# Performance work log

Hardware: AMD Instinct MI355X
Metric: run time of the kernel (lower is better)

The kernel has to match this reference:

```python
import jax, jax.numpy as jnp
import numpy as np

N, E = 16384, 262144
IN, H, OUT = 128, 256, 256
L, HEADS = 4, 8
OC = H // HEADS  # 32, also MHA head_dim
B, NB = 64, 256  # graphs, nodes per graph (N = B*NB, equal-size graphs)


def _ln(x, g, b, eps=1e-5):
    m = x.mean(-1, keepdims=True)
    v = ((x - m) ** 2).mean(-1, keepdims=True)
    return (x - m) / jnp.sqrt(v + eps) * g + b


def setup_inputs() -> dict:
    key = jax.random.key(0)
    ks = iter(jax.random.split(key, 40))
    r = lambda *s: jax.random.normal(next(ks), s, jnp.float32) * 0.05
    return dict(
        x=jax.random.normal(next(ks), (N, IN), jnp.float32),
        edge_index=jax.random.randint(next(ks), (2, E), 0, N),
        wi=r(IN, H), bi=r(H),
        wg=r(L, H, H), asrc=r(L, HEADS, OC), adst=r(L, HEADS, OC), bg=r(L, H),
        g1=jnp.ones((L, H)), b1=jnp.zeros((L, H)),
        inw=r(L, 3 * H, H), inb=r(L, 3 * H), ow=r(L, H, H), ob=r(L, H),
        g2=jnp.ones((L, H)), b2=jnp.zeros((L, H)),
        mw1=r(L, H, 2 * H), mb1=r(L, 2 * H), mw2=r(L, 2 * H, H), mb2=r(L, H),
        g3=jnp.ones((L, H)), b3=jnp.zeros((L, H)),
        gf=jnp.ones(H), bf=jnp.zeros(H),
        wo=r(H, OUT), bo=r(OUT),
    )


def reference(x, edge_index, wi, bi, wg, asrc, adst, bg, g1, b1, inw, inb,
              ow, ob, g2, b2, mw1, mb1, mw2, mb2, g3, b3, gf, bf, wo, bo):
    src, dst = edge_index[0], edge_index[1]
    x = jax.nn.relu(x @ wi + bi)  # [N, H]
    for i in range(L):
        # ---- GATConv (local MPNN), eval mode (no dropout) ----
        xw = (x @ wg[i]).reshape(N, HEADS, OC)
        a = (xw * asrc[i]).sum(-1)[src] + (xw * adst[i]).sum(-1)[dst]  # [E, HEADS]
        a = jax.nn.leaky_relu(a, 0.2)
        amax = jax.ops.segment_max(a, dst, num_segments=N)
        ae = jnp.exp(a - amax[dst])
        asum = jax.ops.segment_sum(ae, dst, num_segments=N)
        attn = ae / asum[dst]  # edge softmax per destination node
        h = jax.ops.segment_sum(attn[:, :, None] * xw[src], dst, num_segments=N)
        h = h.reshape(N, H) + bg[i]
        h = _ln(h + x, g1[i], b1[i])  # GPSConv local branch + residual + norm1
        # ---- global MultiheadAttention over dense batch (equal-size graphs) ----
        xd = x.reshape(B, NB, H)
        qkv = xd @ inw[i].T + inb[i]
        q, k, v = jnp.split(qkv, 3, axis=-1)
        q = q.reshape(B, NB, HEADS, OC).transpose(0, 2, 1, 3)
        k = k.reshape(B, NB, HEADS, OC).transpose(0, 2, 1, 3)
        v = v.reshape(B, NB, HEADS, OC).transpose(0, 2, 1, 3)
        p = jax.nn.softmax(jnp.einsum('bhqd,bhkd->bhqk', q, k) / jnp.sqrt(jnp.float32(OC)), axis=-1)
        o = jnp.einsum('bhqk,bhkd->bhqd', p, v).transpose(0, 2, 1, 3).reshape(B, NB, H)
        o = (o @ ow[i].T + ob[i]).reshape(N, H)
        h2 = _ln(o + x, g2[i], b2[i])  # global branch + residual + norm2
        out = h + h2
        out = out + (jax.nn.relu(out @ mw1[i] + mb1[i]) @ mw2[i] + mb2[i])  # MLP residual
        x = _ln(out, g3[i], b3[i])  # norm3
    x = _ln(x, gf, bf)
    return x @ wo + bo
```

## Files before the change

### kernel.cpp

```cpp
#include <hip/hip_runtime.h>
#include <hip/hip_bf16.h>

#define NNODES 16384
#define NEDGES 262144
#define IND    128
#define HD     256
#define OUTDIM 256
#define LAYERS 4
#define NHEADS 8
#define OCD    32
#define NGRAPH 64
#define NBATCH 256
#define XQSTR  1024

typedef __hip_bfloat16 bf16;
typedef __attribute__((ext_vector_type(8))) short bf16x8;
typedef __attribute__((ext_vector_type(4))) short s16x4;
typedef __attribute__((ext_vector_type(4))) float f32x4;

__device__ __forceinline__ short bfbits(float v) {
    bf16 h = __float2bfloat16(v);
    return *(short*)&h;
}
__device__ __forceinline__ float b2f(short s) {
    return __uint_as_float(((unsigned)(unsigned short)s) << 16);
}

__device__ __forceinline__ void gload_lds16(const short* g, short* l) {
    __builtin_amdgcn_global_load_lds(
        (const __attribute__((address_space(1))) void*)g,
        (__attribute__((address_space(3))) void*)l, 16, 0, 0);
}

__global__ void cvt_kernel(const float* __restrict__ in, short* __restrict__ out, int n)
{
    int i = blockIdx.x * blockDim.x + threadIdx.x;
    if (i < n) out[i] = bfbits(in[i]);
}

__global__ void transpose_cvt_kernel(const float* __restrict__ in, short* __restrict__ out,
                                     int K, int N)
{
    int i = blockIdx.x * blockDim.x + threadIdx.x;
    if (i >= K * N) return;
    const float* ip = in + (size_t)blockIdx.y * K * N;
    short* op = out + (size_t)blockIdx.y * K * N;
    int k = i / N, n = i % N;
    op[(size_t)n * K + k] = bfbits(ip[i]);
}

__global__ void build_wcomb_kernel(const float* __restrict__ inw, const float* __restrict__ wg,
                                   short* __restrict__ wcomb)
{
    int i = blockIdx.x * blockDim.x + threadIdx.x;
    int l = i >> 18, r = (i >> 8) & 1023, k = i & 255;
    float v;
    if (r < 768) v = inw[(size_t)l * 768 * 256 + r * 256 + k];
    else         v = wg[(size_t)l * 256 * 256 + k * 256 + (r - 768)];
    wcomb[i] = bfbits(v);
}

__global__ void build_cbias_kernel(const float* __restrict__ inb, float* __restrict__ cbias)
{
    int i = blockIdx.x * blockDim.x + threadIdx.x;
    int l = i >> 10, c = i & 1023;
    cbias[i] = (c < 768) ? inb[l * 768 + c] : 0.f;
}

__global__ void hist_kernel(const int* __restrict__ dst, int* __restrict__ cnt)
{
    int e = blockIdx.x * blockDim.x + threadIdx.x;
    if (e < NEDGES) atomicAdd(&cnt[dst[e]], 1);
}

__global__ void scan_kernel(const int* __restrict__ cnt, int* __restrict__ row_ptr)
{
    __shared__ int part[256];
    int t = threadIdx.x;
    const int PER = NNODES / 256;
    int base = t * PER;
    int s = 0;
    for (int i = 0; i < PER; i++) s += cnt[base + i];
    part[t] = s;
    __syncthreads();
    for (int off = 1; off < 256; off <<= 1) {
        int v = (t >= off) ? part[t - off] : 0;
        __syncthreads();
        part[t] += v;
        __syncthreads();
    }
    int run = (t == 0) ? 0 : part[t - 1];
    for (int i = 0; i < PER; i++) { row_ptr[base + i] = run; run += cnt[base + i]; }
    if (t == 255) row_ptr[NNODES] = run;
}

__global__ void scatter_kernel(const int* __restrict__ src, const int* __restrict__ dst,
                               const int* __restrict__ row_ptr, int* __restrict__ fill,
                               int* __restrict__ srcs)
{
    int e = blockIdx.x * blockDim.x + threadIdx.x;
    if (e >= NEDGES) return;
    int d = dst[e];
    int pos = row_ptr[d] + atomicAdd(&fill[d], 1);
    srcs[pos] = src[e];
}

__global__ void gat_scores_kernel(const short* __restrict__ xw16,
                                  const float* __restrict__ asrc, const float* __restrict__ adst,
                                  float* __restrict__ ssrc, float* __restrict__ sdst)
{
    int i = blockIdx.x * blockDim.x + threadIdx.x;
    if (i >= NNODES * NHEADS) return;
    int n = i >> 3, h = i & 7;
    const bf16x8* xr = (const bf16x8*)(xw16 + (size_t)n * XQSTR + h * OCD);
    float s1 = 0.f, s2 = 0.f;
#pragma unroll
    for (int g = 0; g < 4; g++) {
        bf16x8 v8 = xr[g];
#pragma unroll
        for (int j = 0; j < 8; j++) {
            float v = b2f(v8[j]);
            int d = g * 8 + j;
            s1 += v * asrc[h * OCD + d];
            s2 += v * adst[h * OCD + d];
        }
    }
    ssrc[i] = s1;
    sdst[i] = s2;
}

__global__ __launch_bounds__(256)
void gat_agg_ln_kernel(const int* __restrict__ row_ptr, const int* __restrict__ srcs,
                       const float* __restrict__ ssrc, const float* __restrict__ sdst,
                       const short* __restrict__ xw16, const float* __restrict__ xcur,
                       const float* __restrict__ colbias, const float* __restrict__ gamma,
                       const float* __restrict__ beta, float* __restrict__ out)
{
    int wave = threadIdx.x >> 6, lane = threadIdx.x & 63;
    int n = blockIdx.x * 4 + wave;
    int c0 = lane << 2;
    int h = c0 >> 5;
    int start = row_ptr[n];
    int deg = row_ptr[n + 1] - start;
    float sd = sdst[n * NHEADS + h];

    float ax = 0.f, ay = 0.f, az = 0.f, aw = 0.f, l = 0.f;
    int j = 0;
    for (; j + 4 <= deg; j += 4) {
        int e0 = srcs[start + j + 0], e1 = srcs[start + j + 1];
        int e2 = srcs[start + j + 2], e3 = srcs[start + j + 3];
        s16x4 r0 = *(const s16x4*)&xw16[(size_t)e0 * XQSTR + c0];
        s16x4 r1 = *(const s16x4*)&xw16[(size_t)e1 * XQSTR + c0];
        s16x4 r2 = *(const s16x4*)&xw16[(size_t)e2 * XQSTR + c0];
        s16x4 r3 = *(const s16x4*)&xw16[(size_t)e3 * XQSTR + c0];
        float a0 = ssrc[e0 * NHEADS + h] + sd; a0 = a0 > 0.f ? a0 : 0.2f * a0;
        float a1 = ssrc[e1 * NHEADS + h] + sd; a1 = a1 > 0.f ? a1 : 0.2f * a1;
        float a2 = ssrc[e2 * NHEADS + h] + sd; a2 = a2 > 0.f ? a2 : 0.2f * a2;
        float a3 = ssrc[e3 * NHEADS + h] + sd; a3 = a3 > 0.f ? a3 : 0.2f * a3;
        float p0 = __expf(a0), p1 = __expf(a1), p2 = __expf(a2), p3 = __expf(a3);
        l += (p0 + p1) + (p2 + p3);
        ax += p0 * b2f(r0[0]) + p1 * b2f(r1[0]) + p2 * b2f(r2[0]) + p3 * b2f(r3[0]);
        ay += p0 * b2f(r0[1]) + p1 * b2f(r1[1]) + p2 * b2f(r2[1]) + p3 * b2f(r3[1]);
        az += p0 * b2f(r0[2]) + p1 * b2f(r1[2]) + p2 * b2f(r2[2]) + p3 * b2f(r3[2]);
        aw += p0 * b2f(r0[3]) + p1 * b2f(r1[3]) + p2 * b2f(r2[3]) + p3 * b2f(r3[3]);
    }
    for (; j < deg; j++) {
        int e0 = srcs[start + j];
        s16x4 r0 = *(const s16x4*)&xw16[(size_t)e0 * XQSTR + c0];
        float a0 = ssrc[e0 * NHEADS + h] + sd; a0 = a0 > 0.f ? a0 : 0.2f * a0;
        float p0 = __expf(a0);
        l += p0;
        ax += p0 * b2f(r0[0]); ay += p0 * b2f(r0[1]);
        az += p0 * b2f(r0[2]); aw += p0 * b2f(r0[3]);
    }
    float invl = deg ? 1.f / l : 0.f;
    size_t base = (size_t)n * HD + c0;
    float4 x4 = *(const float4*)&xcur[base];
    float4 cb = *(const float4*)&colbias[c0];
    float4 v;
    v.x = ax * invl + x4.x + cb.x;
    v.y = ay * invl + x4.y + cb.y;
    v.z = az * invl + x4.z + cb.z;
    v.w = aw * invl + x4.w + cb.w;
    float s = v.x + v.y + v.z + v.w;
    float q = v.x * v.x + v.y * v.y + v.z * v.z + v.w * v.w;
#pragma unroll
    for (int off = 1; off < 64; off <<= 1) {
        s += __shfl_xor(s, off);
        q += __shfl_xor(q, off);
    }
    float mean = s * (1.f / HD);
    float var  = fmaxf(q * (1.f / HD) - mean * mean, 0.f);
    float inv  = rsqrtf(var + 1e-5f);
    float4 g  = *(const float4*)&gamma[c0];
    float4 bt = *(const float4*)&beta[c0];
    float4 y;
    y.x = (v.x - mean) * inv * g.x + bt.x;
    y.y = (v.y - mean) * inv * g.y + bt.y;
    y.z = (v.z - mean) * inv * g.z + bt.z;
    y.w = (v.w - mean) * inv * g.w + bt.w;
    *(float4*)&out[base] = y;
}

#define GBM 128
#define GBK 32

template<int TN>
__global__ __launch_bounds__(256)
void gemm_mfma_kernel(const short* __restrict__ A16, const short* __restrict__ B16,
                      const float* __restrict__ bias, const float* __restrict__ resid,
                      float* __restrict__ Cf, short* __restrict__ C16,
                      int M, int Nc, int K, int relu)
{
    constexpr int NTF = TN / 32;
    __shared__ short As[GBM * GBK];
    __shared__ short Bs[TN * GBK];
    int tid = threadIdx.x;
    int wid = tid >> 6, lane = tid & 63;
    int quad = lane >> 4, l16 = lane & 15;
    int wm = wid >> 1, wn = wid & 1;
    int rowBase = blockIdx.y * GBM;
    int colBase = blockIdx.x * TN;

    f32x4 acc[4][NTF];
#pragma unroll
    for (int mt = 0; mt < 4; mt++)
#pragma unroll
        for (int nt = 0; nt < NTF; nt++) acc[mt][nt] = (f32x4)(0.f);

    int ar  = tid >> 2;
    int akq = (tid & 3) * 8;

    const short* Ag0 = &A16[(size_t)(rowBase + ar) * K + akq];
    const short* Ag1 = &A16[(size_t)(rowBase + ar + 64) * K + akq];
    const short* Bg0 = &B16[(size_t)(colBase + ar) * K + akq];
    const short* Bg1 = (TN == 128) ? &B16[(size_t)(colBase + ar + 64) * K + akq] : nullptr;
    short* AsW0 = As + wid * 512;
    short* AsW1 = As + 64 * GBK + wid * 512;
    short* BsW0 = Bs + wid * 512;
    short* BsW1 = Bs + 64 * GBK + wid * 512;

    for (int k0 = 0; k0 < K; k0 += GBK) {
        gload_lds16(Ag0 + k0, AsW0);
        gload_lds16(Ag1 + k0, AsW1);
        gload_lds16(Bg0 + k0, BsW0);
        if (TN == 128) gload_lds16(Bg1 + k0, BsW1);
        __syncthreads();
        bf16x8 aF[4], bF[NTF];
#pragma unroll
        for (int mt = 0; mt < 4; mt++)
            aF[mt] = *(bf16x8*)&As[(wm * 64 + mt * 16 + l16) * GBK + quad * 8];
#pragma unroll
        for (int nt = 0; nt < NTF; nt++)
            bF[nt] = *(bf16x8*)&Bs[(wn * (TN / 2) + nt * 16 + l16) * GBK + quad * 8];
#pragma unroll
        for (int mt = 0; mt < 4; mt++)
#pragma unroll
            for (int nt = 0; nt < NTF; nt++)
                acc[mt][nt] = __builtin_amdgcn_mfma_f32_16x16x32_bf16(
                    aF[mt], bF[nt], acc[mt][nt], 0, 0, 0);
        __syncthreads();
    }

#pragma unroll
    for (int mt = 0; mt < 4; mt++) {
#pragma unroll
        for (int nt = 0; nt < NTF; nt++) {
            int col = colBase + wn * (TN / 2) + nt * 16 + l16;
            float bv = bias ? bias[col] : 0.f;
#pragma unroll
            for (int r = 0; r < 4; r++) {
                int row = rowBase + wm * 64 + mt * 16 + quad * 4 + r;
                float v = acc[mt][nt][r] + bv;
                if (resid) v += resid[(size_t)row * Nc + col];
                if (relu)  v = fmaxf(v, 0.f);
                if (Cf)  Cf[(size_t)row * Nc + col] = v;
                if (C16) C16[(size_t)row * Nc + col] = bfbits(v);
            }
        }
    }
}

__global__ __launch_bounds__(256)
void ln4_kernel(const float* __restrict__ in, const float* __restrict__ res,
                const float* __restrict__ gamma, const float* __restrict__ beta,
                const float* __restrict__ postadd,
                float* __restrict__ outf, short* __restrict__ out16)
{
    int wave = threadIdx.x >> 6, lane = threadIdx.x & 63;
    int row = blockIdx.x * 4 + wave;
    size_t base = (size_t)row * HD + lane * 4;
    float4 v = *(const float4*)&in[base];
    if (res) {
        float4 r = *(const float4*)&res[base];
        v.x += r.x; v.y += r.y; v.z += r.z; v.w += r.w;
    }
    float s = v.x + v.y + v.z + v.w;
    float q = v.x * v.x + v.y * v.y + v.z * v.z + v.w * v.w;
#pragma unroll
    for (int off = 1; off < 64; off <<= 1) {
        s += __shfl_xor(s, off);
        q += __shfl_xor(q, off);
    }
    float mean = s * (1.f / HD);
    float var  = fmaxf(q * (1.f / HD) - mean * mean, 0.f);
    float inv  = rsqrtf(var + 1e-5f);
    float4 g  = *(const float4*)&gamma[lane * 4];
    float4 bt = *(const float4*)&beta[lane * 4];
    float4 y;
    y.x = (v.x - mean) * inv * g.x + bt.x;
    y.y = (v.y - mean) * inv * g.y + bt.y;
    y.z = (v.z - mean) * inv * g.z + bt.z;
    y.w = (v.w - mean) * inv * g.w + bt.w;
    if (postadd) {
        float4 p = *(const float4*)&postadd[base];
        y.x += p.x; y.y += p.y; y.z += p.z; y.w += p.w;
    }
    if (outf) *(float4*)&outf[base] = y;
    if (out16) {
        s16x4 o;
        o[0] = bfbits(y.x); o[1] = bfbits(y.y); o[2] = bfbits(y.z); o[3] = bfbits(y.w);
        *(s16x4*)&out16[base] = o;
    }
}

#define PSTR 72
__global__ __launch_bounds__(256)
void mha_mfma_kernel(const short* __restrict__ qkv16, short* __restrict__ o16)
{
    __shared__ short smem[4 * 64 * PSTR + 32 * PSTR];
    short* VT = smem + 4 * 64 * PSTR;

    int b = blockIdx.x, h = blockIdx.y;
    int tid = threadIdx.x;
    int wid = tid >> 6, lane = tid & 63;
    int quad = lane >> 4, l16 = lane & 15;
    int base = b * NBATCH;
    int qrow0 = wid * 64;
    short* Pme = smem + wid * 64 * PSTR;

    const float scale2 = 0.17677669529663687f * 1.4426950408889634f;

    bf16x8 qA[4];
#pragma unroll
    for (int mt = 0; mt < 4; mt++)
        qA[mt] = *(const bf16x8*)&qkv16[(size_t)(base + qrow0 + mt * 16 + l16) * XQSTR + h * 32 + quad * 8];

    f32x4 accO[4][2];
#pragma unroll
    for (int mt = 0; mt < 4; mt++)
#pragma unroll
        for (int dt = 0; dt < 2; dt++) accO[mt][dt] = (f32x4)(0.f);
    float lsum[4][4];
#pragma unroll
    for (int mt = 0; mt < 4; mt++)
#pragma unroll
        for (int r = 0; r < 4; r++) lsum[mt][r] = 0.f;

    for (int c = 0; c < 4; c++) {
        __syncthreads();
        {
            int key = tid >> 2, dq = (tid & 3) * 8;
            bf16x8 v = *(const bf16x8*)&qkv16[(size_t)(base + c * 64 + key) * XQSTR + 512 + h * 32 + dq];
#pragma unroll
            for (int j = 0; j < 8; j++) VT[(dq + j) * PSTR + key] = v[j];
        }
        __syncthreads();
        bf16x8 kB[4];
#pragma unroll
        for (int kt = 0; kt < 4; kt++)
            kB[kt] = *(const bf16x8*)&qkv16[(size_t)(base + c * 64 + kt * 16 + l16) * XQSTR + 256 + h * 32 + quad * 8];
#pragma unroll
        for (int mt = 0; mt < 4; mt++) {
#pragma unroll
            for (int kt = 0; kt < 4; kt++) {
                f32x4 s = __builtin_amdgcn_mfma_f32_16x16x32_bf16(qA[mt], kB[kt], (f32x4)(0.f), 0, 0, 0);
#pragma unroll
                for (int r = 0; r < 4; r++) {
                    float p = exp2f(s[r] * scale2);
                    lsum[mt][r] += p;
                    Pme[(mt * 16 + quad * 4 + r) * PSTR + kt * 16 + l16] = bfbits(p);
                }
            }
        }
        __syncthreads();
#pragma unroll
        for (int mt = 0; mt < 4; mt++) {
#pragma unroll
            for (int ks = 0; ks < 2; ks++) {
                bf16x8 pA = *(bf16x8*)&Pme[(mt * 16 + l16) * PSTR + ks * 32 + quad * 8];
#pragma unroll
                for (int dt = 0; dt < 2; dt++) {
                    bf16x8 vB = *(bf16x8*)&VT[(dt * 16 + l16) * PSTR + ks * 32 + quad * 8];
                    accO[mt][dt] = __builtin_amdgcn_mfma_f32_16x16x32_bf16(pA, vB, accO[mt][dt], 0, 0, 0);
                }
            }
        }
    }
#pragma unroll
    for (int mt = 0; mt < 4; mt++)
#pragma unroll
        for (int r = 0; r < 4; r++) {
            float v = lsum[mt][r];
            v += __shfl_xor(v, 1);
            v += __shfl_xor(v, 2);
            v += __shfl_xor(v, 4);
            v += __shfl_xor(v, 8);
            lsum[mt][r] = v;
        }
#pragma unroll
    for (int mt = 0; mt < 4; mt++)
#pragma unroll
        for (int dt = 0; dt < 2; dt++)
#pragma unroll
            for (int r = 0; r < 4; r++) {
                int row = base + qrow0 + mt * 16 + quad * 4 + r;
                int col = h * 32 + dt * 16 + l16;
                o16[(size_t)row * HD + col] = bfbits(accO[mt][dt][r] / lsum[mt][r]);
            }
}

extern "C" void kernel_launch(void* const* d_in, const int* in_sizes, int n_in,
                              void* d_out, int out_size, void* d_ws, size_t ws_size,
                              hipStream_t stream)
{
    const float* x0   = (const float*)d_in[0];
    const int*   ei   = (const int*)d_in[1];
    const float* wi   = (const float*)d_in[2];
    const float* bi   = (const float*)d_in[3];
    const float* wg   = (const float*)d_in[4];
    const float* asrc = (const float*)d_in[5];
    const float* adst = (const float*)d_in[6];
    const float* bg   = (const float*)d_in[7];
    const float* g1   = (const float*)d_in[8];
    const float* b1   = (const float*)d_in[9];
    const float* inw  = (const float*)d_in[10];
    const float* inb  = (const float*)d_in[11];
    const float* ow   = (const float*)d_in[12];
    const float* ob   = (const float*)d_in[13];
    const float* g2   = (const float*)d_in[14];
    const float* b2   = (const float*)d_in[15];
    const float* mw1  = (const float*)d_in[16];
    const float* mb1  = (const float*)d_in[17];
    const float* mw2  = (const float*)d_in[18];
    const float* mb2  = (const float*)d_in[19];
    const float* g3   = (const float*)d_in[20];
    const float* b3   = (const float*)d_in[21];
    const float* gf   = (const float*)d_in[22];
    const float* bf_  = (const float*)d_in[23];
    const float* wo   = (const float*)d_in[24];
    const float* bo   = (const float*)d_in[25];

    const int* srcI = ei;
    const int* dstI = ei + NEDGES;

    const size_t NH = (size_t)NNODES * HD;
    float* ws   = (float*)d_ws;
    float* xcur = ws;
    float* xw   = xcur + NH;
    float* hbuf = xw + NH;
    float* obuf = hbuf + NH;
    float* qkvb = obuf + NH;
    int*   srcs    = (int*)(qkvb + 3 * NH);
    int*   row_ptr = srcs + NEDGES;
    int*   cnt     = row_ptr + NNODES + 1;
    int*   fill    = cnt + NNODES;
    float* ssrc    = (float*)(fill + NNODES);
    float* sdst    = ssrc + (size_t)NNODES * NHEADS;
    short* xq16   = (short*)qkvb;
    short* x016   = (short*)(sdst + (size_t)NNODES * NHEADS);
    short* xcur16 = x016 + (size_t)NNODES * IND;
    short* b16a   = xcur16 + NH;
    short* hid16  = b16a + NH;
    short* wi_t  = hid16 + 2 * NH;
    short* wcomb = wi_t + (size_t)HD * IND;
    short* ow_c  = wcomb + (size_t)LAYERS * 1024 * HD;
    short* mw1_t = ow_c + (size_t)LAYERS * HD * HD;
    short* mw2_t = mw1_t + (size_t)LAYERS * HD * 2 * HD;
    short* wo_t  = mw2_t + (size_t)LAYERS * 2 * HD * HD;
    float* cbias = (float*)(wo_t + (size_t)HD * OUTDIM);

    const int T = 256;
    const int nNH = NNODES * NHEADS;

    cvt_kernel<<<(NNODES * IND + T - 1) / T, T, 0, stream>>>(x0, x016, NNODES * IND);
    transpose_cvt_kernel<<<dim3((IND * HD + T - 1) / T, 1), T, 0, stream>>>(wi, wi_t, IND, HD);
    build_wcomb_kernel<<<(LAYERS * 1024 * HD) / T, T, 0, stream>>>(inw, wg, wcomb);
    build_cbias_kernel<<<(LAYERS * 1024) / T, T, 0, stream>>>(inb, cbias);
    cvt_kernel<<<(LAYERS * HD * HD + T - 1) / T, T, 0, stream>>>(ow, ow_c, LAYERS * HD * HD);
    transpose_cvt_kernel<<<dim3((HD * 2 * HD + T - 1) / T, LAYERS), T, 0, stream>>>(mw1, mw1_t, HD, 2 * HD);
    transpose_cvt_kernel<<<dim3((2 * HD * HD + T - 1) / T, LAYERS), T, 0, stream>>>(mw2, mw2_t, 2 * HD, HD);
    transpose_cvt_kernel<<<dim3((HD * OUTDIM + T - 1) / T, 1), T, 0, stream>>>(wo, wo_t, HD, OUTDIM);

    hipMemsetAsync(cnt, 0, NNODES * sizeof(int), stream);
    hipMemsetAsync(fill, 0, NNODES * sizeof(int), stream);
    hist_kernel<<<(NEDGES + T - 1) / T, T, 0, stream>>>(dstI, cnt);
    scan_kernel<<<1, 256, 0, stream>>>(cnt, row_ptr);
    scatter_kernel<<<(NEDGES + T - 1) / T, T, 0, stream>>>(srcI, dstI, row_ptr, fill, srcs);

    gemm_mfma_kernel<64><<<dim3(HD / 64, NNODES / GBM), 256, 0, stream>>>(
        x016, wi_t, bi, nullptr, xcur, xcur16, NNODES, HD, IND, 1);

    for (int i = 0; i < LAYERS; i++) {
        const float* asrc_i = asrc + (size_t)i * NHEADS * OCD;
        const float* adst_i = adst + (size_t)i * NHEADS * OCD;
        const float* bg_i   = bg + (size_t)i * HD;
        const float* g1_i   = g1 + (size_t)i * HD;
        const float* b1_i   = b1 + (size_t)i * HD;
        const float* ob_i   = ob + (size_t)i * HD;
        const float* g2_i   = g2 + (size_t)i * HD;
        const float* b2_i   = b2 + (size_t)i * HD;
        const float* mb1_i  = mb1 + (size_t)i * 2 * HD;
        const float* mb2_i  = mb2 + (size_t)i * HD;
        const float* g3_i   = g3 + (size_t)i * HD;
        const float* b3_i   = b3 + (size_t)i * HD;
        const short* wcomb_i = wcomb + (size_t)i * 1024 * HD;
        const float* cbias_i = cbias + (size_t)i * 1024;
        const short* ow_ci  = ow_c + (size_t)i * HD * HD;
        const short* mw1_ti = mw1_t + (size_t)i * HD * 2 * HD;
        const short* mw2_ti = mw2_t + (size_t)i * 2 * HD * HD;

        gemm_mfma_kernel<128><<<dim3(1024 / 128, NNODES / GBM), 256, 0, stream>>>(
            xcur16, wcomb_i, cbias_i, nullptr, nullptr, xq16, NNODES, 1024, HD, 0);

        gat_scores_kernel<<<(nNH + T - 1) / T, T, 0, stream>>>(xq16 + 768, asrc_i, adst_i, ssrc, sdst);
        gat_agg_ln_kernel<<<NNODES / 4, 256, 0, stream>>>(
            row_ptr, srcs, ssrc, sdst, xq16 + 768, xcur, bg_i, g1_i, b1_i, hbuf);

        mha_mfma_kernel<<<dim3(NGRAPH, NHEADS), 256, 0, stream>>>(xq16, b16a);
        gemm_mfma_kernel<64><<<dim3(HD / 64, NNODES / GBM), 256, 0, stream>>>(
            b16a, ow_ci, ob_i, nullptr, xw, nullptr, NNODES, HD, HD, 0);
        ln4_kernel<<<NNODES / 4, 256, 0, stream>>>(xw, xcur, g2_i, b2_i, hbuf, obuf, b16a);

        gemm_mfma_kernel<128><<<dim3(2 * HD / 128, NNODES / GBM), 256, 0, stream>>>(
            b16a, mw1_ti, mb1_i, nullptr, nullptr, hid16, NNODES, 2 * HD, HD, 1);
        gemm_mfma_kernel<64><<<dim3(HD / 64, NNODES / GBM), 256, 0, stream>>>(
            hid16, mw2_ti, mb2_i, obuf, xw, nullptr, NNODES, HD, 2 * HD, 0);
        ln4_kernel<<<NNODES / 4, 256, 0, stream>>>(xw, nullptr, g3_i, b3_i, nullptr, xcur, xcur16);
    }

    ln4_kernel<<<NNODES / 4, 256, 0, stream>>>(xcur, nullptr, gf, bf_, nullptr, nullptr, b16a);
    gemm_mfma_kernel<64><<<dim3(OUTDIM / 64, NNODES / GBM), 256, 0, stream>>>(
        b16a, wo_t, bo, nullptr, (float*)d_out, nullptr, NNODES, OUTDIM, HD, 0);
}
```

Measured before the change: 879.3 us.

## Fuse output-projection and MLP-down GEMMs with LayerNorm epilogue, vectorize GEMM stores

```diff
diff --git a/kernel.cpp b/kernel.cpp
--- a/kernel.cpp
+++ b/kernel.cpp
@@ -258,25 +258,158 @@
 #pragma unroll
             for (int nt = 0; nt < NTF; nt++)
                 acc[mt][nt] = __builtin_amdgcn_mfma_f32_16x16x32_bf16(
-                    aF[mt], bF[nt], acc[mt][nt], 0, 0, 0);
+                    bF[nt], aF[mt], acc[mt][nt], 0, 0, 0);
         __syncthreads();
     }
 
 #pragma unroll
     for (int mt = 0; mt < 4; mt++) {
+        int row = rowBase + wm * 64 + mt * 16 + l16;
 #pragma unroll
         for (int nt = 0; nt < NTF; nt++) {
-            int col = colBase + wn * (TN / 2) + nt * 16 + l16;
-            float bv = bias ? bias[col] : 0.f;
-#pragma unroll
-            for (int r = 0; r < 4; r++) {
-                int row = rowBase + wm * 64 + mt * 16 + quad * 4 + r;
-                float v = acc[mt][nt][r] + bv;
-                if (resid) v += resid[(size_t)row * Nc + col];
-                if (relu)  v = fmaxf(v, 0.f);
-                if (Cf)  Cf[(size_t)row * Nc + col] = v;
-                if (C16) C16[(size_t)row * Nc + col] = bfbits(v);
-            }
+            int col0 = colBase + wn * (TN / 2) + nt * 16 + quad * 4;
+            f32x4 v = acc[mt][nt];
+            if (bias) {
+                float4 b4 = *(const float4*)&bias[col0];
+                v[0] += b4.x; v[1] += b4.y; v[2] += b4.z; v[3] += b4.w;
+            }
+            if (resid) {
+                float4 r4 = *(const float4*)&resid[(size_t)row * Nc + col0];
+                v[0] += r4.x; v[1] += r4.y; v[2] += r4.z; v[3] += r4.w;
+            }
+            if (relu) {
+                v[0] = fmaxf(v[0], 0.f); v[1] = fmaxf(v[1], 0.f);
+                v[2] = fmaxf(v[2], 0.f); v[3] = fmaxf(v[3], 0.f);
+            }
+            if (Cf) {
+                float4 o; o.x = v[0]; o.y = v[1]; o.z = v[2]; o.w = v[3];
+                *(float4*)&Cf[(size_t)row * Nc + col0] = o;
+            }
+            if (C16) {
+                s16x4 o;
+                o[0] = bfbits(v[0]); o[1] = bfbits(v[1]);
+                o[2] = bfbits(v[2]); o[3] = bfbits(v[3]);
+                *(s16x4*)&C16[(size_t)row * Nc + col0] = o;
+            }
+        }
+    }
+}
+
+__global__ __launch_bounds__(256)
+void gemm_ln_kernel(const short* __restrict__ A16, const short* __restrict__ B16,
+                    const float* __restrict__ bias, const float* __restrict__ resid,
+                    const float* __restrict__ gamma, const float* __restrict__ beta,
+                    const float* __restrict__ postadd,
+                    float* __restrict__ outf, short* __restrict__ out16, int K)
+{
+    __shared__ short As[GBM * GBK];
+    __shared__ short Bs[256 * GBK];
+    __shared__ float sred_s[2][GBM];
+    __shared__ float sred_q[2][GBM];
+    int tid = threadIdx.x;
+    int wid = tid >> 6, lane = tid & 63;
+    int quad = lane >> 4, l16 = lane & 15;
+    int wm = wid >> 1, wn = wid & 1;
+    int rowBase = blockIdx.y * GBM;
+
+    f32x4 acc[4][8];
+#pragma unroll
+    for (int mt = 0; mt < 4; mt++)
+#pragma unroll
+        for (int nt = 0; nt < 8; nt++) acc[mt][nt] = (f32x4)(0.f);
+
+    int ar  = tid >> 2;
+    int akq = (tid & 3) * 8;
+
+    const short* Ag0 = &A16[(size_t)(rowBase + ar) * K + akq];
+    const short* Ag1 = &A16[(size_t)(rowBase + ar + 64) * K + akq];
+    const short* Bg0 = &B16[(size_t)(ar) * K + akq];
+    const short* Bg1 = &B16[(size_t)(ar + 64) * K + akq];
+    const short* Bg2 = &B16[(size_t)(ar + 128) * K + akq];
+    const short* Bg3 = &B16[(size_t)(ar + 192) * K + akq];
+    short* AsW0 = As + wid * 512;
+    short* AsW1 = As + 64 * GBK + wid * 512;
+    short* BsW0 = Bs + wid * 512;
+    short* BsW1 = Bs + 64 * GBK + wid * 512;
+    short* BsW2 = Bs + 128 * GBK + wid * 512;
+    short* BsW3 = Bs + 192 * GBK + wid * 512;
+
+    for (int k0 = 0; k0 < K; k0 += GBK) {
+        gload_lds16(Ag0 + k0, AsW0);
+        gload_lds16(Ag1 + k0, AsW1);
+        gload_lds16(Bg0 + k0, BsW0);
+        gload_lds16(Bg1 + k0, BsW1);
+        gload_lds16(Bg2 + k0, BsW2);
+        gload_lds16(Bg3 + k0, BsW3);
+        __syncthreads();
+        bf16x8 aF[4], bF[8];
+#pragma unroll
+        for (int mt = 0; mt < 4; mt++)
+            aF[mt] = *(bf16x8*)&As[(wm * 64 + mt * 16 + l16) * GBK + quad * 8];
+#pragma unroll
+        for (int nt = 0; nt < 8; nt++)
+            bF[nt] = *(bf16x8*)&Bs[(wn * 128 + nt * 16 + l16) * GBK + quad * 8];
+#pragma unroll
+        for (int mt = 0; mt < 4; mt++)
+#pragma unroll
+            for (int nt = 0; nt < 8; nt++)
+                acc[mt][nt] = __builtin_amdgcn_mfma_f32_16x16x32_bf16(
+                    bF[nt], aF[mt], acc[mt][nt], 0, 0, 0);
+        __syncthreads();
+    }
+
+#pragma unroll
+    for (int mt = 0; mt < 4; mt++) {
+        int row = rowBase + wm * 64 + mt * 16 + l16;
+        float s = 0.f, q = 0.f;
+#pragma unroll
+        for (int nt = 0; nt < 8; nt++) {
+            int col0 = wn * 128 + nt * 16 + quad * 4;
+            f32x4 v = acc[mt][nt];
+            float4 b4 = *(const float4*)&bias[col0];
+            float4 r4 = *(const float4*)&resid[(size_t)row * HD + col0];
+            v[0] += b4.x + r4.x; v[1] += b4.y + r4.y;
+            v[2] += b4.z + r4.z; v[3] += b4.w + r4.w;
+            acc[mt][nt] = v;
+            s += (v[0] + v[1]) + (v[2] + v[3]);
+            q += (v[0] * v[0] + v[1] * v[1]) + (v[2] * v[2] + v[3] * v[3]);
+        }
+        s += __shfl_xor(s, 16); s += __shfl_xor(s, 32);
+        q += __shfl_xor(q, 16); q += __shfl_xor(q, 32);
+        if (quad == 0) {
+            sred_s[wn][wm * 64 + mt * 16 + l16] = s;
+            sred_q[wn][wm * 64 + mt * 16 + l16] = q;
+        }
+    }
+    __syncthreads();
+#pragma unroll
+    for (int mt = 0; mt < 4; mt++) {
+        int rowl = wm * 64 + mt * 16 + l16;
+        int row = rowBase + rowl;
+        float s = sred_s[0][rowl] + sred_s[1][rowl];
+        float q = sred_q[0][rowl] + sred_q[1][rowl];
+        float mean = s * (1.f / HD);
+        float var  = fmaxf(q * (1.f / HD) - mean * mean, 0.f);
+        float inv  = rsqrtf(var + 1e-5f);
+#pragma unroll
+        for (int nt = 0; nt < 8; nt++) {
+            int col0 = wn * 128 + nt * 16 + quad * 4;
+            f32x4 v = acc[mt][nt];
+            float4 g4 = *(const float4*)&gamma[col0];
+            float4 bt = *(const float4*)&beta[col0];
+            float4 y;
+            y.x = (v[0] - mean) * inv * g4.x + bt.x;
+            y.y = (v[1] - mean) * inv * g4.y + bt.y;
+            y.z = (v[2] - mean) * inv * g4.z + bt.z;
+            y.w = (v[3] - mean) * inv * g4.w + bt.w;
+            if (postadd) {
+                float4 p4 = *(const float4*)&postadd[(size_t)row * HD + col0];
+                y.x += p4.x; y.y += p4.y; y.z += p4.z; y.w += p4.w;
+            }
+            *(float4*)&outf[(size_t)row * HD + col0] = y;
+            s16x4 o;
+            o[0] = bfbits(y.x); o[1] = bfbits(y.y); o[2] = bfbits(y.z); o[3] = bfbits(y.w);
+            *(s16x4*)&out16[(size_t)row * HD + col0] = o;
         }
     }
 }
@@ -528,15 +661,13 @@
             row_ptr, srcs, ssrc, sdst, xq16 + 768, xcur, bg_i, g1_i, b1_i, hbuf);
 
         mha_mfma_kernel<<<dim3(NGRAPH, NHEADS), 256, 0, stream>>>(xq16, b16a);
-        gemm_mfma_kernel<64><<<dim3(HD / 64, NNODES / GBM), 256, 0, stream>>>(
-            b16a, ow_ci, ob_i, nullptr, xw, nullptr, NNODES, HD, HD, 0);
-        ln4_kernel<<<NNODES / 4, 256, 0, stream>>>(xw, xcur, g2_i, b2_i, hbuf, obuf, b16a);
+        gemm_ln_kernel<<<dim3(1, NNODES / GBM), 256, 0, stream>>>(
+            b16a, ow_ci, ob_i, xcur, g2_i, b2_i, hbuf, obuf, b16a, HD);
 
         gemm_mfma_kernel<128><<<dim3(2 * HD / 128, NNODES / GBM), 256, 0, stream>>>(
             b16a, mw1_ti, mb1_i, nullptr, nullptr, hid16, NNODES, 2 * HD, HD, 1);
-        gemm_mfma_kernel<64><<<dim3(HD / 64, NNODES / GBM), 256, 0, stream>>>(
-            hid16, mw2_ti, mb2_i, obuf, xw, nullptr, NNODES, HD, 2 * HD, 0);
-        ln4_kernel<<<NNODES / 4, 256, 0, stream>>>(xw, nullptr, g3_i, b3_i, nullptr, xcur, xcur16);
+        gemm_ln_kernel<<<dim3(1, NNODES / GBM), 256, 0, stream>>>(
+            hid16, mw2_ti, mb2_i, obuf, g3_i, b3_i, nullptr, xcur, xcur16, 2 * HD);
     }
 
     ln4_kernel<<<NNODES / 4, 256, 0, stream>>>(xcur, nullptr, gf, bf_, nullptr, nullptr, b16a);
```

After: 892.7 us. No clear change (+1.5%).
